# Optimization experiments

Hardware: AMD Instinct MI355X
Metric: run time of the kernel (lower is better)

The kernel has to match this reference:

```python
import jax, jax.numpy as jnp
import numpy as np

B = 64
T0_V = 512   # existing timesteps already in the graph memory
TAU_V = 128  # new timesteps inserted this call
NTOT = T0_V + TAU_V  # 640 == graph_size
FEAT = 256
K = 16       # causal temporal window (edges j->i for j in [i-K, i))


def _build_edges():
    # per-batch causal edges, then offset by b*NTOT into the flat graph
    src_l, dst_l = [], []
    for off in range(1, K + 1):
        ii = np.arange(off, NTOT)
        src_l.append(ii - off)
        dst_l.append(ii)
    src = np.concatenate(src_l)
    dst = np.concatenate(dst_l)
    boff = (np.arange(B) * NTOT)[:, None]
    edge_src = (src[None, :] + boff).reshape(-1)
    edge_dst = (dst[None, :] + boff).reshape(-1)
    return jnp.asarray(edge_src, jnp.int32), jnp.asarray(edge_dst, jnp.int32)


def setup_inputs() -> dict:
    key = jax.random.key(0)
    ks = jax.random.split(key, 8)
    x = jax.random.normal(ks[0], (B, TAU_V, FEAT), jnp.float32)
    nodes = 0.1 * jax.random.normal(ks[1], (B, NTOT, FEAT), jnp.float32)
    edge_src, edge_dst = _build_edges()
    E = edge_src.shape[0]
    edge_weight = jnp.ones((E,), jnp.float32)
    sc = 1.0 / np.sqrt(FEAT)
    W1_self = sc * jax.random.normal(ks[2], (FEAT, FEAT), jnp.float32)
    W1_nbr = sc * jax.random.normal(ks[3], (FEAT, FEAT), jnp.float32)
    b1 = jnp.zeros((FEAT,), jnp.float32)
    W2_self = sc * jax.random.normal(ks[4], (FEAT, FEAT), jnp.float32)
    W2_nbr = sc * jax.random.normal(ks[5], (FEAT, FEAT), jnp.float32)
    b2 = jnp.zeros((FEAT,), jnp.float32)
    return {"x": x, "nodes": nodes, "edge_weight": edge_weight,
            "W1_self": W1_self, "W1_nbr": W1_nbr, "b1": b1,
            "W2_self": W2_self, "W2_nbr": W2_nbr, "b2": b2,
            "edge_src": edge_src, "edge_dst": edge_dst,
            "T0": T0_V, "tau": TAU_V}


def reference(x, nodes, edge_weight, W1_self, W1_nbr, b1, W2_self, W2_nbr, b2,
              edge_src, edge_dst, T0, tau):
    Bv, t, feat = x.shape
    ntot = T0 + tau
    # scatter new observations into the node memory (uniform taus -> dense slice)
    nodes = nodes.at[:, T0:T0 + tau, :].set(x)
    # adj normalization: values / values.detach() == 1 in the forward pass
    w = edge_weight / jax.lax.stop_gradient(edge_weight)
    # flatten per-batch ragged graphs (regular here since taus are uniform)
    flat = nodes[:, :ntot].reshape(Bv * ntot, feat)  # [B*ntot, feat]
    nseg = Bv * ntot

    def gconv(h, Ws, Wn, b):
        msg = h[edge_src] * w[:, None]                       # [E, d] gather
        agg = jax.ops.segment_sum(msg, edge_dst, num_segments=nseg)
        return jnp.tanh(h @ Ws + agg @ Wn + b)

    h = gconv(flat, W1_self, W1_nbr, b1)
    h = gconv(h, W2_self, W2_nbr, b2)
    # gather outputs for the newly-inserted nodes -> [B, tau, out_feat]
    out_idx = (jnp.arange(Bv)[:, None] * ntot + T0 + jnp.arange(tau)[None, :]).reshape(-1)
    mx_dense = h[out_idx].reshape(Bv, tau, -1)
    return mx_dense
```

## Files before the change

### kernel.cpp

```cpp
#include <hip/hip_runtime.h>
#include <hip/hip_bf16.h>


namespace {

constexpr int BQ    = 64;
constexpr int FEATC = 256;
constexpr int M1 = 144;
constexpr int M2 = 128;

using ushort = unsigned short;
using short8 = __attribute__((ext_vector_type(8))) short;
using f32x4  = __attribute__((ext_vector_type(4))) float;

__device__ __forceinline__ ushort f2bf(float f) {
  union { float f; unsigned u; } v{f};
  unsigned r = v.u + 0x7FFFu + ((v.u >> 16) & 1u);
  return (ushort)(r >> 16);
}
__device__ __forceinline__ float bf2f(ushort h) {
  union { unsigned u; float f; } v{(unsigned)h << 16};
  return v.f;
}
__device__ __forceinline__ void split2(float v, ushort& hi, ushort& lo) {
  hi = f2bf(v);
  lo = f2bf(v - bf2f(hi));
}
__device__ __forceinline__ float tanh_fast(float x) {
  const float e = __builtin_amdgcn_exp2f(x * 2.8853900817779268f);
  return 1.0f - 2.0f * __builtin_amdgcn_rcpf(1.0f + e);
}
__device__ __forceinline__ void gl_lds16(const ushort* g, ushort* l) {
  __builtin_amdgcn_global_load_lds(
      (const __attribute__((address_space(1))) void*)g,
      (__attribute__((address_space(3))) void*)l, 16, 0, 0);
}

__device__ __forceinline__ size_t frag_idx(int row, int k, int s) {
  return ((size_t)(((row >> 4) * 16 + (k >> 5)) * 2 + s)) * 512
       + ((k >> 3) & 3) * 128 + (row & 15) * 8 + (k & 7);
}
__device__ __forceinline__ int lofs(int row_l, int k, int s) {
  return ((k >> 5) * 2 + s) * 512 + ((k >> 3) & 3) * 128 + row_l * 8 + (k & 7);
}

__global__ __launch_bounds__(256) void prep_fused(
    const float* __restrict__ x, const float* __restrict__ nodes,
    const float* __restrict__ W1s, const float* __restrict__ W1n,
    const float* __restrict__ W2s, const float* __restrict__ W2n,
    ushort* __restrict__ A1F, ushort* __restrict__ WF1,
    ushort* __restrict__ WF2) {
  __shared__ ushort lds_o[16384];
  __shared__ float tile[64][65];
  const int blk = blockIdx.x;
  if (blk < 576) {
    const int G = 4 * (blk % 144) + (blk / 144);
    const int b = G / 9, c = G % 9, f = threadIdx.x;
    const int t0 = c * 16, i0 = 496 + t0;
    const float* nb = nodes + ((size_t)b * 640) * FEATC + f;
    const float* xb = x     + ((size_t)b * 128) * FEATC + f;

    float v[32];
    #pragma unroll
    for (int d = 0; d < 32; ++d) {
      const int i = i0 - 16 + d;
      v[d] = (i < 512) ? nb[(size_t)i * FEATC] : xb[(size_t)(i - 512) * FEATC];
    }
    float win = 0.f;
    #pragma unroll
    for (int d = 0; d < 16; ++d) win += v[d];

    #pragma unroll
    for (int tt = 0; tt < 16; ++tt) {
      ushort hi, lo;
      split2(v[16 + tt], hi, lo);
      lds_o[lofs(tt, f, 0)] = hi;
      lds_o[lofs(tt, f, 1)] = lo;
      split2(win, hi, lo);
      lds_o[lofs(tt, 256 + f, 0)] = hi;
      lds_o[lofs(tt, 256 + f, 1)] = lo;
      win += v[16 + tt] - v[tt];
    }
    __syncthreads();
    ushort* dst = A1F + (size_t)G * 16384;
    #pragma unroll
    for (int it = 0; it < 8; ++it) {
      const int idx = it * 256 + threadIdx.x;
      *(short8*)(dst + idx * 8) = *(const short8*)(lds_o + idx * 8);
    }
  } else {
    const int w = blk - 576;
    const int z = w >> 4, rem = w & 15;
    const int k0 = (rem >> 2) * 64, n0 = (rem & 3) * 64;
    const float* src = (z == 0) ? W1s : (z == 1) ? W1n : (z == 2) ? W2s : W2n;
    ushort* dst = (z < 2) ? WF1 : WF2;
    const int koff = (z & 1) * 256;
    const int c = threadIdx.x & 63, r4 = threadIdx.x >> 6;
    #pragma unroll
    for (int p = 0; p < 16; ++p) {
      const int k = r4 + p * 4;
      tile[k][c] = src[(size_t)(k0 + k) * FEATC + n0 + c];
    }
    __syncthreads();
    #pragma unroll
    for (int p = 0; p < 16; ++p) {
      const int n = r4 + p * 4;
      ushort hi, lo;
      split2(tile[c][n], hi, lo);
      dst[frag_idx(n0 + n, koff + k0 + c, 0)] = hi;
      dst[frag_idx(n0 + n, koff + k0 + c, 1)] = lo;
    }
  }
}

#define GLOAD(dst, ptr)                                                      \
  asm volatile("global_load_dwordx4 %0, %1, off"                             \
               : "=v"(dst) : "v"(ptr) : "memory")

#define WAITV(n) do {                                                        \
  asm volatile("s_waitcnt vmcnt(" #n ")" ::: "memory");                      \
  __builtin_amdgcn_sched_barrier(0);                                         \
} while (0)

#define MF(a, b, c) c = __builtin_amdgcn_mfma_f32_16x16x32_bf16(a, b, c, 0, 0, 0)

#define STAGEA(jn, kb) do {                                                  \
  gl_lds16(srcu0 + (kb) * 1024, sbase + (jn) * 5120 + u0 * 512);             \
  gl_lds16(srcu1 + (kb) * 1024, sbase + (jn) * 5120 + u1 * 512);             \
  if (g3) gl_lds16(srcu2 + (kb) * 1024, sbase + (jn) * 5120 + u2 * 512);     \
} while (0)

#define WAITW do { if (g3) { WAITV(5); } else { WAITV(4); } } while (0)

#define COMPJ2(j, WH, WL) do {                                               \
  const ushort* bp_ = sbase + (j) * 5120 + lane * 8;                         \
  const short8 a0h = *(const short8*)(bp_ + 0 * 512);                        \
  const short8 a0l = *(const short8*)(bp_ + 1 * 512);                        \
  const short8 a1h = *(const short8*)(bp_ + 2 * 512);                        \
  const short8 a1l = *(const short8*)(bp_ + 3 * 512);                        \
  const short8 a2h = *(const short8*)(bp_ + 4 * 512);                        \
  const short8 a2l = *(const short8*)(bp_ + 5 * 512);                        \
  const short8 a3h = *(const short8*)(bp_ + 6 * 512);                        \
  const short8 a3l = *(const short8*)(bp_ + 7 * 512);                        \
  const short8 a4h = *(const short8*)(bp_ + 8 * 512);                        \
  const short8 a4l = *(const short8*)(bp_ + 9 * 512);                        \
  __builtin_amdgcn_s_setprio(1);                                            \
  MF(a0h, WH, acc[0]); MF(a1h, WH, acc[1]); MF(a2h, WH, acc[2]);             \
  MF(a3h, WH, acc[3]); MF(a4h, WH, acc[4]);                                  \
  MF(a0h, WL, acc[0]); MF(a1h, WL, acc[1]); MF(a2h, WL, acc[2]);             \
  MF(a3h, WL, acc[3]); MF(a4h, WL, acc[4]);                                  \
  MF(a0l, WH, acc[0]); MF(a1l, WH, acc[1]); MF(a2l, WH, acc[2]);             \
  MF(a3l, WH, acc[3]); MF(a4l, WH, acc[4]);                                  \
  __builtin_amdgcn_s_setprio(0);                                            \
  __builtin_amdgcn_sched_barrier(0);                                        \
} while (0)

__global__ __launch_bounds__(256, 2) void gemm1_fused(
    const ushort* __restrict__ A, const ushort* __restrict__ W,
    const float* __restrict__ bias, ushort* __restrict__ A2F) {
  __shared__ __align__(16) unsigned char ldsmem[54528];
  ushort* sbase = (ushort*)ldsmem;
  float (*hvt)[68] = (float(*)[68])ldsmem;
  ushort* outb = (ushort*)(ldsmem + 21760);

  const int tid = threadIdx.x;
  const int wave = tid >> 6, lane = tid & 63;
  const int lr = lane & 15, kg = lane >> 4;
  const int mx2 = blockIdx.x, ny = blockIdx.y;
  const int b = mx2 >> 1, half = mx2 & 1;
  const int rgA0 = 9 * b + 4 * half;
  const int n0 = ny * 64;
  const int ngw = ny * 4 + wave;

  const bool g3 = (wave < 2);
  const int uw = g3 ? wave * 3 : 6 + (wave - 2) * 2;
  const int u0 = uw, u1 = uw + 1, u2 = g3 ? uw + 2 : uw + 1;
  auto srcA = [&](int u) {
    return A + ((size_t)(rgA0 + (u >> 1)) * 32 + (u & 1)) * 512 + lane * 8;
  };
  const ushort* srcu0 = srcA(u0);
  const ushort* srcu1 = srcA(u1);
  const ushort* srcu2 = srcA(u2);

  const ushort* bW = W + (size_t)ngw * 16384 + lane * 8;

  f32x4 acc[5] = {};
  short8 w0h, w0l, w1h, w1l, w2h, w2l;

  STAGEA(0, 0); GLOAD(w0h, bW);        GLOAD(w0l, bW + 512);
  STAGEA(1, 1); GLOAD(w1h, bW + 1024); GLOAD(w1l, bW + 1536);

#define STEP(k, j, jn, WH, WL, NWH, NWL)                                     \
  WAITW; __builtin_amdgcn_s_barrier();                                       \
  COMPJ2(j, WH, WL);                                                         \
  STAGEA(jn, (k) + 2);                                                       \
  GLOAD(NWH, bW + ((k) + 2) * 1024); GLOAD(NWL, bW + ((k) + 2) * 1024 + 512)

  STEP(0, 0, 2, w0h, w0l, w2h, w2l);
  STEP(1, 1, 0, w1h, w1l, w0h, w0l);
  STEP(2, 2, 1, w2h, w2l, w1h, w1l);
  STEP(3, 0, 2, w0h, w0l, w2h, w2l);
  STEP(4, 1, 0, w1h, w1l, w0h, w0l);
  STEP(5, 2, 1, w2h, w2l, w1h, w1l);
  STEP(6, 0, 2, w0h, w0l, w2h, w2l);
  STEP(7, 1, 0, w1h, w1l, w0h, w0l);
  STEP(8, 2, 1, w2h, w2l, w1h, w1l);
  STEP(9, 0, 2, w0h, w0l, w2h, w2l);
  STEP(10, 1, 0, w1h, w1l, w0h, w0l);
  STEP(11, 2, 1, w2h, w2l, w1h, w1l);
  STEP(12, 0, 2, w0h, w0l, w2h, w2l);
  STEP(13, 1, 0, w1h, w1l, w0h, w0l);
  WAITW; __builtin_amdgcn_s_barrier();
  COMPJ2(2, w2h, w2l);
  WAITV(0); __builtin_amdgcn_s_barrier();
  COMPJ2(0, w0h, w0l);
#undef STEP

  __syncthreads();

  const float bv = bias[n0 + wave * 16 + lr];
  #pragma unroll
  for (int fr = 0; fr < 5; ++fr)
    #pragma unroll
    for (int r = 0; r < 4; ++r)
      hvt[fr * 16 + kg * 4 + r][wave * 16 + lr] = tanh_fast(acc[fr][r] + bv);
  __syncthreads();

  {
    const int col = tid & 63, q = tid >> 6;
    float hv[32];
    #pragma unroll
    for (int d = 0; d < 32; ++d) hv[d] = hvt[q * 16 + d][col];
    float win = 0.f;
    #pragma unroll
    for (int d = 0; d < 16; ++d) win += hv[d];

    const int su = ((q * 4 + (col >> 5)) * 2) * 512
                 + ((col >> 3) & 3) * 128 + (col & 7);
    const int wu = ((q * 4 + 2 + (col >> 5)) * 2) * 512
                 + ((col >> 3) & 3) * 128 + (col & 7);
    #pragma unroll
    for (int tt = 0; tt < 16; ++tt) {
      ushort hi, lo;
      split2(hv[16 + tt], hi, lo);
      outb[su + tt * 8]       = hi;
      outb[su + tt * 8 + 512] = lo;
      split2(win, hi, lo);
      outb[wu + tt * 8]       = hi;
      outb[wu + tt * 8 + 512] = lo;
      win += hv[16 + tt] - hv[tt];
    }
  }
  __syncthreads();

  const int rg20 = 4 * mx2;
  #pragma unroll
  for (int it = 0; it < 8; ++it) {
    const int lin = it * 2048 + tid * 8;
    const int u = lin >> 9, w = lin & 511;
    const int uq = u >> 3, ukbl = (u >> 1) & 3, us = u & 1;
    const int KB = (ukbl < 2) ? (2 * ny + ukbl) : (8 + 2 * ny + (ukbl - 2));
    const size_t dst = ((size_t)((rg20 + uq) * 16 + KB) * 2 + us) * 512 + w;
    *(short8*)(A2F + dst) = *(const short8*)(outb + lin);
  }
}

#define STAGE2(jn, kb) do {                                                  \
  gl_lds16(srcv0 + (kb) * 1024, sb2 + (jn) * 4096 + v0 * 512);               \
  gl_lds16(srcv1 + (kb) * 1024, sb2 + (jn) * 4096 + v1 * 512);               \
} while (0)

#define COMPK(j, WH, WL) do {                                                \
  const ushort* bp_ = sb2 + (j) * 4096 + lane * 8;                           \
  const short8 a0h = *(const short8*)(bp_ + 0 * 512);                        \
  const short8 a0l = *(const short8*)(bp_ + 1 * 512);                        \
  const short8 a1h = *(const short8*)(bp_ + 2 * 512);                        \
  const short8 a1l = *(const short8*)(bp_ + 3 * 512);                        \
  const short8 a2h = *(const short8*)(bp_ + 4 * 512);                        \
  const short8 a2l = *(const short8*)(bp_ + 5 * 512);                        \
  const short8 a3h = *(const short8*)(bp_ + 6 * 512);                        \
  const short8 a3l = *(const short8*)(bp_ + 7 * 512);                        \
  __builtin_amdgcn_s_setprio(1);                                            \
  MF(a0h, WH, acc[0]); MF(a1h, WH, acc[1]);                                  \
  MF(a2h, WH, acc[2]); MF(a3h, WH, acc[3]);                                  \
  MF(a0h, WL, acc[0]); MF(a1h, WL, acc[1]);                                  \
  MF(a2h, WL, acc[2]); MF(a3h, WL, acc[3]);                                  \
  MF(a0l, WH, acc[0]); MF(a1l, WH, acc[1]);                                  \
  MF(a2l, WH, acc[2]); MF(a3l, WH, acc[3]);                                  \
  __builtin_amdgcn_s_setprio(0);                                            \
  __builtin_amdgcn_sched_barrier(0);                                        \
} while (0)

__global__ __launch_bounds__(256, 2) void gemm2_lds(
    const ushort* __restrict__ A, const ushort* __restrict__ W,
    const float* __restrict__ bias, float* __restrict__ out) {
  __shared__ __align__(16) ushort sb2[3 * 4096];

  const int tid = threadIdx.x;
  const int wave = tid >> 6, lane = tid & 63;
  const int lr = lane & 15, kg = lane >> 4;
  const int mx = blockIdx.x, ny = blockIdx.y;
  const int rg0 = mx * 4;
  const int ngw = ny * 4 + wave;
  const int n0col = ngw * 16;

  const int v0 = wave * 2, v1 = wave * 2 + 1;
  auto srcA = [&](int u) {
    return A + ((size_t)(rg0 + (u >> 1)) * 32 + (u & 1)) * 512 + lane * 8;
  };
  const ushort* srcv0 = srcA(v0);
  const ushort* srcv1 = srcA(v1);
  const ushort* bW = W + (size_t)ngw * 16384 + lane * 8;

  f32x4 acc[4] = {};
  short8 w0h, w0l, w1h, w1l, w2h, w2l;

  STAGE2(0, 0); GLOAD(w0h, bW);        GLOAD(w0l, bW + 512);
  STAGE2(1, 1); GLOAD(w1h, bW + 1024); GLOAD(w1l, bW + 1536);

#define STEP2(k, j, jn, WH, WL, NWH, NWL)                                    \
  WAITV(4); __builtin_amdgcn_s_barrier();                                    \
  COMPK(j, WH, WL);                                                          \
  STAGE2(jn, (k) + 2);                                                       \
  GLOAD(NWH, bW + ((k) + 2) * 1024); GLOAD(NWL, bW + ((k) + 2) * 1024 + 512)

  STEP2(0, 0, 2, w0h, w0l, w2h, w2l);
  STEP2(1, 1, 0, w1h, w1l, w0h, w0l);
  STEP2(2, 2, 1, w2h, w2l, w1h, w1l);
  STEP2(3, 0, 2, w0h, w0l, w2h, w2l);
  STEP2(4, 1, 0, w1h, w1l, w0h, w0l);
  STEP2(5, 2, 1, w2h, w2l, w1h, w1l);
  STEP2(6, 0, 2, w0h, w0l, w2h, w2l);
  STEP2(7, 1, 0, w1h, w1l, w0h, w0l);
  STEP2(8, 2, 1, w2h, w2l, w1h, w1l);
  STEP2(9, 0, 2, w0h, w0l, w2h, w2l);
  STEP2(10, 1, 0, w1h, w1l, w0h, w0l);
  STEP2(11, 2, 1, w2h, w2l, w1h, w1l);
  STEP2(12, 0, 2, w0h, w0l, w2h, w2l);
  STEP2(13, 1, 0, w1h, w1l, w0h, w0l);
  WAITV(4); __builtin_amdgcn_s_barrier();
  COMPK(2, w2h, w2l);
  WAITV(0); __builtin_amdgcn_s_barrier();
  COMPK(0, w0h, w0l);
#undef STEP2

  const float bv = bias[n0col + lr];
  #pragma unroll
  for (int fr = 0; fr < 4; ++fr)
    #pragma unroll
    for (int r = 0; r < 4; ++r) {
      const int row = mx * 64 + fr * 16 + kg * 4 + r;
      out[(size_t)row * FEATC + n0col + lr] = tanh_fast(acc[fr][r] + bv);
    }
}

}

extern "C" void kernel_launch(void* const* d_in, const int* in_sizes, int n_in,
                              void* d_out, int out_size, void* d_ws, size_t ws_size,
                              hipStream_t stream) {
  const float* x     = (const float*)d_in[0];
  const float* nodes = (const float*)d_in[1];
  const float* W1s = (const float*)d_in[3];
  const float* W1n = (const float*)d_in[4];
  const float* b1  = (const float*)d_in[5];
  const float* W2s = (const float*)d_in[6];
  const float* W2n = (const float*)d_in[7];
  const float* b2  = (const float*)d_in[8];
  float* out = (float*)d_out;

  const size_t a1_sz = (size_t)BQ * M1 * 1024;
  const size_t a2_sz = (size_t)BQ * M2 * 1024;
  const size_t wf_sz = (size_t)16 * 16 * 2 * 512;
  const size_t need = (a1_sz + a2_sz + 2 * wf_sz) * sizeof(ushort);
  if (ws_size < need) return;

  ushort* p = (ushort*)d_ws;
  ushort* A1F = p; p += a1_sz;
  ushort* A2F = p; p += a2_sz;
  ushort* WF1 = p; p += wf_sz;
  ushort* WF2 = p; p += wf_sz;

  prep_fused<<<640, 256, 0, stream>>>(x, nodes, W1s, W1n, W2s, W2n,
                                      A1F, WF1, WF2);
  gemm1_fused<<<dim3(BQ * 2, FEATC / 64), 256, 0, stream>>>(A1F, WF1, b1, A2F);
  gemm2_lds<<<dim3((BQ * M2) / 64, FEATC / 64), 256, 0, stream>>>(
      A2F, WF2, b2, out);
}
```

Before: 35.77 us.

## Deepen GEMM prefetch to five buffers and coalesce gemm2 output stores

```diff
diff --git a/kernel.cpp b/kernel.cpp
--- a/kernel.cpp
+++ b/kernel.cpp
@@ -130,7 +130,7 @@
   if (g3) gl_lds16(srcu2 + (kb) * 1024, sbase + (jn) * 5120 + u2 * 512);     \
 } while (0)
 
-#define WAITW do { if (g3) { WAITV(5); } else { WAITV(4); } } while (0)
+#define WAITW1 do { if (g3) { WAITV(5); } else { WAITV(4); } } while (0)
 
 #define COMPJ2(j, WH, WL) do {                                               \
   const ushort* bp_ = sbase + (j) * 5120 + lane * 8;                         \
@@ -155,6 +155,12 @@
   __builtin_amdgcn_sched_barrier(0);                                        \
 } while (0)
 
+#define HALF1(j, ks, js, WH, WL, NWH, NWL) do {                              \
+  COMPJ2(j, WH, WL);                                                         \
+  STAGEA(js, ks);                                                            \
+  GLOAD(NWH, bW + (ks) * 1024); GLOAD(NWL, bW + (ks) * 1024 + 512);          \
+} while (0)
+
 __global__ __launch_bounds__(256, 2) void gemm1_fused(
     const ushort* __restrict__ A, const ushort* __restrict__ W,
     const float* __restrict__ bias, ushort* __restrict__ A2F) {
@@ -185,36 +191,28 @@
   const ushort* bW = W + (size_t)ngw * 16384 + lane * 8;
 
   f32x4 acc[5] = {};
-  short8 w0h, w0l, w1h, w1l, w2h, w2l;
+  short8 w0h, w0l, w1h, w1l, w2h, w2l, w3h, w3l, w4h, w4l;
 
   STAGEA(0, 0); GLOAD(w0h, bW);        GLOAD(w0l, bW + 512);
   STAGEA(1, 1); GLOAD(w1h, bW + 1024); GLOAD(w1l, bW + 1536);
-
-#define STEP(k, j, jn, WH, WL, NWH, NWL)                                     \
-  WAITW; __builtin_amdgcn_s_barrier();                                       \
-  COMPJ2(j, WH, WL);                                                         \
-  STAGEA(jn, (k) + 2);                                                       \
-  GLOAD(NWH, bW + ((k) + 2) * 1024); GLOAD(NWL, bW + ((k) + 2) * 1024 + 512)
-
-  STEP(0, 0, 2, w0h, w0l, w2h, w2l);
-  STEP(1, 1, 0, w1h, w1l, w0h, w0l);
-  STEP(2, 2, 1, w2h, w2l, w1h, w1l);
-  STEP(3, 0, 2, w0h, w0l, w2h, w2l);
-  STEP(4, 1, 0, w1h, w1l, w0h, w0l);
-  STEP(5, 2, 1, w2h, w2l, w1h, w1l);
-  STEP(6, 0, 2, w0h, w0l, w2h, w2l);
-  STEP(7, 1, 0, w1h, w1l, w0h, w0l);
-  STEP(8, 2, 1, w2h, w2l, w1h, w1l);
-  STEP(9, 0, 2, w0h, w0l, w2h, w2l);
-  STEP(10, 1, 0, w1h, w1l, w0h, w0l);
-  STEP(11, 2, 1, w2h, w2l, w1h, w1l);
-  STEP(12, 0, 2, w0h, w0l, w2h, w2l);
-  STEP(13, 1, 0, w1h, w1l, w0h, w0l);
-  WAITW; __builtin_amdgcn_s_barrier();
-  COMPJ2(2, w2h, w2l);
+  STAGEA(2, 2); GLOAD(w2h, bW + 2048); GLOAD(w2l, bW + 2560);
+
+  WAITW1; __builtin_amdgcn_s_barrier();
+  HALF1(0, 3, 3, w0h, w0l, w3h, w3l);  HALF1(1, 4, 4, w1h, w1l, w4h, w4l);
+  WAITW1; __builtin_amdgcn_s_barrier();
+  HALF1(2, 5, 0, w2h, w2l, w0h, w0l);  HALF1(3, 6, 1, w3h, w3l, w1h, w1l);
+  WAITW1; __builtin_amdgcn_s_barrier();
+  HALF1(4, 7, 2, w4h, w4l, w2h, w2l);  HALF1(0, 8, 3, w0h, w0l, w3h, w3l);
+  WAITW1; __builtin_amdgcn_s_barrier();
+  HALF1(1, 9, 4, w1h, w1l, w4h, w4l);  HALF1(2, 10, 0, w2h, w2l, w0h, w0l);
+  WAITW1; __builtin_amdgcn_s_barrier();
+  HALF1(3, 11, 1, w3h, w3l, w1h, w1l); HALF1(4, 12, 2, w4h, w4l, w2h, w2l);
+  WAITW1; __builtin_amdgcn_s_barrier();
+  HALF1(0, 13, 3, w0h, w0l, w3h, w3l); HALF1(1, 14, 4, w1h, w1l, w4h, w4l);
+  WAITW1; __builtin_amdgcn_s_barrier();
+  HALF1(2, 15, 0, w2h, w2l, w0h, w0l); COMPJ2(3, w3h, w3l);
   WAITV(0); __builtin_amdgcn_s_barrier();
-  COMPJ2(0, w0h, w0l);
-#undef STEP
+  COMPJ2(4, w4h, w4l); COMPJ2(0, w0h, w0l);
 
   __syncthreads();
 
@@ -291,17 +289,25 @@
   __builtin_amdgcn_sched_barrier(0);                                        \
 } while (0)
 
+#define HALF2(j, ks, js, WH, WL, NWH, NWL) do {                              \
+  COMPK(j, WH, WL);                                                          \
+  STAGE2(js, ks);                                                            \
+  GLOAD(NWH, bW + (ks) * 1024); GLOAD(NWL, bW + (ks) * 1024 + 512);          \
+} while (0)
+
 __global__ __launch_bounds__(256, 2) void gemm2_lds(
     const ushort* __restrict__ A, const ushort* __restrict__ W,
     const float* __restrict__ bias, float* __restrict__ out) {
-  __shared__ __align__(16) ushort sb2[3 * 4096];
+  __shared__ __align__(16) unsigned char lds2[40960];
+  ushort* sb2 = (ushort*)lds2;
+  float (*tile)[68] = (float(*)[68])lds2;
 
   const int tid = threadIdx.x;
   const int wave = tid >> 6, lane = tid & 63;
   const int lr = lane & 15, kg = lane >> 4;
-  const int mx = blockIdx.x, ny = blockIdx.y;
+  const int mx = blockIdx.x, ny2 = blockIdx.y;
   const int rg0 = mx * 4;
-  const int ngw = ny * 4 + wave;
+  const int ngw = ny2 * 4 + wave;
   const int n0col = ngw * 16;
 
   const int v0 = wave * 2, v1 = wave * 2 + 1;
@@ -313,45 +319,44 @@
   const ushort* bW = W + (size_t)ngw * 16384 + lane * 8;
 
   f32x4 acc[4] = {};
-  short8 w0h, w0l, w1h, w1l, w2h, w2l;
+  short8 w0h, w0l, w1h, w1l, w2h, w2l, w3h, w3l, w4h, w4l;
 
   STAGE2(0, 0); GLOAD(w0h, bW);        GLOAD(w0l, bW + 512);
   STAGE2(1, 1); GLOAD(w1h, bW + 1024); GLOAD(w1l, bW + 1536);
-
-#define STEP2(k, j, jn, WH, WL, NWH, NWL)                                    \
-  WAITV(4); __builtin_amdgcn_s_barrier();                                    \
-  COMPK(j, WH, WL);                                                          \
-  STAGE2(jn, (k) + 2);                                                       \
-  GLOAD(NWH, bW + ((k) + 2) * 1024); GLOAD(NWL, bW + ((k) + 2) * 1024 + 512)
-
-  STEP2(0, 0, 2, w0h, w0l, w2h, w2l);
-  STEP2(1, 1, 0, w1h, w1l, w0h, w0l);
-  STEP2(2, 2, 1, w2h, w2l, w1h, w1l);
-  STEP2(3, 0, 2, w0h, w0l, w2h, w2l);
-  STEP2(4, 1, 0, w1h, w1l, w0h, w0l);
-  STEP2(5, 2, 1, w2h, w2l, w1h, w1l);
-  STEP2(6, 0, 2, w0h, w0l, w2h, w2l);
-  STEP2(7, 1, 0, w1h, w1l, w0h, w0l);
-  STEP2(8, 2, 1, w2h, w2l, w1h, w1l);
-  STEP2(9, 0, 2, w0h, w0l, w2h, w2l);
-  STEP2(10, 1, 0, w1h, w1l, w0h, w0l);
-  STEP2(11, 2, 1, w2h, w2l, w1h, w1l);
-  STEP2(12, 0, 2, w0h, w0l, w2h, w2l);
-  STEP2(13, 1, 0, w1h, w1l, w0h, w0l);
-  WAITV(4); __builtin_amdgcn_s_barrier();
-  COMPK(2, w2h, w2l);
+  STAGE2(2, 2); GLOAD(w2h, bW + 2048); GLOAD(w2l, bW + 2560);
+
+  WAITV(4); __builtin_amdgcn_s_barrier();
+  HALF2(0, 3, 3, w0h, w0l, w3h, w3l);  HALF2(1, 4, 4, w1h, w1l, w4h, w4l);
+  WAITV(4); __builtin_amdgcn_s_barrier();
+  HALF2(2, 5, 0, w2h, w2l, w0h, w0l);  HALF2(3, 6, 1, w3h, w3l, w1h, w1l);
+  WAITV(4); __builtin_amdgcn_s_barrier();
+  HALF2(4, 7, 2, w4h, w4l, w2h, w2l);  HALF2(0, 8, 3, w0h, w0l, w3h, w3l);
+  WAITV(4); __builtin_amdgcn_s_barrier();
+  HALF2(1, 9, 4, w1h, w1l, w4h, w4l);  HALF2(2, 10, 0, w2h, w2l, w0h, w0l);
+  WAITV(4); __builtin_amdgcn_s_barrier();
+  HALF2(3, 11, 1, w3h, w3l, w1h, w1l); HALF2(4, 12, 2, w4h, w4l, w2h, w2l);
+  WAITV(4); __builtin_amdgcn_s_barrier();
+  HALF2(0, 13, 3, w0h, w0l, w3h, w3l); HALF2(1, 14, 4, w1h, w1l, w4h, w4l);
+  WAITV(4); __builtin_amdgcn_s_barrier();
+  HALF2(2, 15, 0, w2h, w2l, w0h, w0l); COMPK(3, w3h, w3l);
   WAITV(0); __builtin_amdgcn_s_barrier();
-  COMPK(0, w0h, w0l);
-#undef STEP2
-
+  COMPK(4, w4h, w4l); COMPK(0, w0h, w0l);
+
+  __syncthreads();
   const float bv = bias[n0col + lr];
   #pragma unroll
   for (int fr = 0; fr < 4; ++fr)
     #pragma unroll
-    for (int r = 0; r < 4; ++r) {
-      const int row = mx * 64 + fr * 16 + kg * 4 + r;
-      out[(size_t)row * FEATC + n0col + lr] = tanh_fast(acc[fr][r] + bv);
-    }
+    for (int r = 0; r < 4; ++r)
+      tile[fr * 16 + kg * 4 + r][wave * 16 + lr] = tanh_fast(acc[fr][r] + bv);
+  __syncthreads();
+  #pragma unroll
+  for (int it = 0; it < 4; ++it) {
+    const int idx = it * 256 + tid;
+    const int row = idx >> 4, ch = idx & 15;
+    *(f32x4*)(out + (size_t)(mx * 64 + row) * FEATC + ny2 * 64 + ch * 4) =
+        *(const f32x4*)&tile[row][ch * 4];
+  }
 }
 
 }
```

Measured after the change: 36.06 us. Within noise of the previous version (+0.8%).
